# Kernel tuning notes

Hardware: AMD Instinct MI355X
Metric: run time of the kernel (lower is better)

## Reference

```python
import jax, jax.numpy as jnp
import numpy as np

EPS = 1e-12  # tf.nn.l2_normalize epsilon


def setup_inputs() -> dict:
    key = jax.random.key(0)
    ks = jax.random.split(key, 6)
    B, S, K, D = 256, 512, 20, 256
    encoded_sents = jax.random.normal(ks[0], (B, S, D), dtype=jnp.float32)
    mask = jax.random.randint(ks[1], (B, S), 0, 2) > 0
    keys = jax.random.normal(ks[2], (B, K, D), dtype=jnp.float32)
    scale = 0.05  # truncated-normal-ish init scale for stability
    U = jax.random.normal(ks[3], (D, D), dtype=jnp.float32) * scale
    V = jax.random.normal(ks[4], (D, D), dtype=jnp.float32) * scale
    W = jax.random.normal(ks[5], (D, D), dtype=jnp.float32) * scale
    return {"encoded_sents": encoded_sents, "mask": mask, "keys": keys,
            "U": U, "V": V, "W": W}


def reference(encoded_sents, mask, keys, U, V, W):
    # encoded_sents: [B,S,D], mask: [B,S] bool, keys: [B,K,D], U/V/W: [D,D]
    kV = jnp.einsum('bkd,de->bke', keys, V)  # time-invariant, hoisted

    def step(h, xm):
        x, m = xm                                   # x: [B,D], m: [B] bool
        # gate: sigmoid(sum_d x*(h+k))  -> [B,K]
        g = jax.nn.sigmoid(jnp.einsum('bd,bkd->bk', x, h + keys))
        # candidate: relu(hU + kV + xW)  -> [B,K,D]
        h_tilda = jax.nn.relu(jnp.einsum('bkd,de->bke', h, U) + kV
                              + (x @ W)[:, None, :])
        upd = h + g[..., None] * h_tilda
        # l2 normalize along dim (tf.nn.l2_normalize semantics)
        sq = jnp.sum(upd * upd, axis=2, keepdims=True)
        upd = upd * jax.lax.rsqrt(jnp.maximum(sq, EPS))
        h_new = jnp.where(m[:, None, None], upd, h)
        return h_new, None

    h0 = jnp.zeros_like(keys)
    xs = (jnp.swapaxes(encoded_sents, 0, 1), mask.T)  # [S,B,D], [S,B]
    hT, _ = jax.lax.scan(step, h0, xs)
    return hT  # [B,K,D]
```

## Files before the change

### kernel.cpp

```cpp
#include <hip/hip_runtime.h>
#include <math.h>

#define B_ 256
#define S_ 512
#define K_ 20
#define D_ 256
#define NT 512
#define LDH 264

typedef __attribute__((ext_vector_type(8))) short short8;
typedef __attribute__((ext_vector_type(4))) float f32x4;
typedef __attribute__((ext_vector_type(8))) _Float16 half8;
typedef __attribute__((ext_vector_type(2))) __fp16 fp16x2;
typedef __attribute__((ext_vector_type(2))) unsigned int uint2v;

__device__ __forceinline__ unsigned short rne_bf16(float f) {
  unsigned u = __builtin_bit_cast(unsigned, f);
  u += 0x7FFFu + ((u >> 16) & 1u);
  return (unsigned short)(u >> 16);
}
__device__ __forceinline__ float bf16_to_f32(unsigned short h) {
  return __builtin_bit_cast(float, ((unsigned)h) << 16);
}
__device__ __forceinline__ unsigned pk_f16(float a, float b) {
  fp16x2 p = __builtin_amdgcn_cvt_pkrtz(a, b);
  return __builtin_bit_cast(unsigned, p);
}

__global__ __launch_bounds__(NT, 2)
void rnn_fused14(const float* __restrict__ es, const int* __restrict__ mask,
                 const float* __restrict__ keys, const float* __restrict__ U,
                 const float* __restrict__ V, const float* __restrict__ W,
                 float* __restrict__ XWc, float* __restrict__ out) {
  __shared__ unsigned short sH0[32 * LDH];
  __shared__ unsigned short sH1[32 * LDH];
  __shared__ float sRed[2][2][32][13];
  __shared__ float sXK[512 * 20 + 16];
  __shared__ short sAct[S_];
  __shared__ int   sNact;

  const int b = blockIdx.x, t = threadIdx.x;
  const int w = t >> 6, lane = t & 63, quad = lane >> 4, n = lane & 15;
  const int e0a = (w << 5) + quad * 4;

  for (int i = t; i < 2 * 2 * 32 * 13; i += NT) ((float*)sRed)[i] = 0.0f;
  if (w == 0) {
    int base = 0;
    for (int c = 0; c < 8; ++c) {
      int s = c * 64 + lane;
      int mv = mask[b * S_ + s];
      unsigned long long bal = __ballot(mv != 0);
      int pos = base + (int)__popcll(bal & ((1ull << lane) - 1ull));
      if (mv) sAct[pos] = (short)s;
      base += (int)__popcll(bal);
    }
    if (lane == 0) sNact = base;
  }
  __syncthreads();
  const int nAct = sNact;

  short8 aHi[8][2], aLo[8][2];
  auto load_A = [&](const float* __restrict__ M) {
#pragma unroll
    for (int kt = 0; kt < 8; ++kt)
#pragma unroll
      for (int et = 0; et < 2; ++et) {
        const int e = ((2 * w + et) << 4) + n;
        const int d0 = kt * 32 + quad * 8;
        short8 h8, l8;
#pragma unroll
        for (int j = 0; j < 8; ++j) {
          float f = M[(d0 + j) * D_ + e];
          unsigned short hi = rne_bf16(f);
          h8[j] = (short)hi;
          l8[j] = (short)rne_bf16(f - bf16_to_f32(hi));
        }
        aHi[kt][et] = h8; aLo[kt][et] = l8;
      }
  };
  auto load_A_keys = [&]() {
#pragma unroll
    for (int kt = 0; kt < 8; ++kt)
#pragma unroll
      for (int et = 0; et < 2; ++et) {
        const int kk2 = ((2 * w + et) << 4) + n;
        const int d0 = kt * 32 + quad * 8;
        short8 h8 = {}, l8 = {};
        if (kk2 < K_) {
#pragma unroll
          for (int j = 0; j < 8; ++j) {
            float f = keys[(size_t)(b * K_ + kk2) * D_ + d0 + j];
            unsigned short hi = rne_bf16(f);
            h8[j] = (short)hi;
            l8[j] = (short)rne_bf16(f - bf16_to_f32(hi));
          }
        }
        aHi[kt][et] = h8; aLo[kt][et] = l8;
      }
  };
  auto run_mfma3 = [&](f32x4 acc[2][2]) {
#pragma unroll
    for (int kt = 0; kt < 8; ++kt) {
      short8 bhi[2], blo[2];
#pragma unroll
      for (int ke = 0; ke < 2; ++ke) {
        const int off = (ke * 16 + n) * LDH + kt * 32 + quad * 8;
        bhi[ke] = *(const short8*)&sH0[off];
        blo[ke] = *(const short8*)&sH1[off];
      }
#pragma unroll
      for (int et = 0; et < 2; ++et)
#pragma unroll
        for (int ke = 0; ke < 2; ++ke) {
          acc[et][ke] = __builtin_amdgcn_mfma_f32_16x16x32_bf16(aHi[kt][et], bhi[ke], acc[et][ke], 0, 0, 0);
          acc[et][ke] = __builtin_amdgcn_mfma_f32_16x16x32_bf16(aLo[kt][et], bhi[ke], acc[et][ke], 0, 0, 0);
          acc[et][ke] = __builtin_amdgcn_mfma_f32_16x16x32_bf16(aHi[kt][et], blo[ke], acc[et][ke], 0, 0, 0);
        }
    }
  };
  auto stage_rows = [&](int p) {
    const int rr = t >> 4, c0 = (t & 15) * 16;
    const int ridx = p * 32 + rr;
    const int sidx = sAct[(ridx < nAct) ? ridx : (nAct - 1)];
    const float* src = es + ((size_t)b * S_ + sidx) * D_ + c0;
#pragma unroll
    for (int h2 = 0; h2 < 2; ++h2) {
      f32x4 f0 = *(const f32x4*)(src + h2 * 8);
      f32x4 f1 = *(const f32x4*)(src + h2 * 8 + 4);
      short8 hh, ll;
#pragma unroll
      for (int j = 0; j < 4; ++j) {
        unsigned short a = rne_bf16(f0[j]);
        hh[j] = (short)a; ll[j] = (short)rne_bf16(f0[j] - bf16_to_f32(a));
        unsigned short bq = rne_bf16(f1[j]);
        hh[4 + j] = (short)bq; ll[4 + j] = (short)rne_bf16(f1[j] - bf16_to_f32(bq));
      }
      *(short8*)&sH0[rr * LDH + c0 + h2 * 8] = hh;
      *(short8*)&sH1[rr * LDH + c0 + h2 * 8] = ll;
    }
  };

  const size_t bbase = (size_t)b * S_;
  const int nPass = (nAct + 31) >> 5;

  if (nAct > 0) {
    load_A_keys();
    for (int p = 0; p < nPass; ++p) {
      stage_rows(p);
      __syncthreads();
      if (w == 0) {
        f32x4 axk[2][2] = {};
        run_mfma3(axk);
#pragma unroll
        for (int et = 0; et < 2; ++et) {
          const int kb = et * 16 + quad * 4;
          if (kb < K_) {
#pragma unroll
            for (int ke = 0; ke < 2; ++ke) {
              const int row = p * 32 + ke * 16 + n;
              *(f32x4*)&sXK[row * 20 + kb] = axk[et][ke];
            }
          }
        }
      }
      __syncthreads();
    }
  }

  if (nAct > 0) {
    load_A(W);
    for (int p = 0; p < nPass; ++p) {
      stage_rows(p);
      __syncthreads();
      f32x4 acc[2][2] = {};
      run_mfma3(acc);
#pragma unroll
      for (int et = 0; et < 2; ++et)
#pragma unroll
        for (int ke = 0; ke < 2; ++ke) {
          const int g = p * 32 + ke * 16 + n;
          if (g < nAct)
            *(f32x4*)&XWc[(bbase + g) * D_ + e0a + 16 * et] = acc[et][ke];
        }
      __syncthreads();
    }
  }

  for (int i = t; i < 32 * LDH; i += NT) { sH0[i] = 0; sH1[i] = 0; }
  __syncthreads();

  for (int i = t; i < K_ * D_; i += NT) {
    int k = i >> 8, d = i & 255;
    float f = keys[(b * K_ + k) * D_ + d];
    unsigned short hi = rne_bf16(f);
    sH0[k * LDH + d] = hi;
    sH1[k * LDH + d] = rne_bf16(f - bf16_to_f32(hi));
  }
  load_A(V);
  __syncthreads();

  f32x4 kvReg[2][2] = {};
  run_mfma3(kvReg);
  __syncthreads();

  for (int i = t; i < K_ * LDH; i += NT) { sH0[i] = 0; sH1[i] = 0; }
  short8 aU[8][2];
#pragma unroll
  for (int kt = 0; kt < 8; ++kt)
#pragma unroll
    for (int et = 0; et < 2; ++et) {
      const int e = ((2 * w + et) << 4) + n;
      const int d0 = kt * 32 + quad * 8;
      short8 h8;
#pragma unroll
      for (int j = 0; j < 8; ++j)
        h8[j] = (short)__builtin_bit_cast(unsigned short, (_Float16)U[(d0 + j) * D_ + e]);
      aU[kt][et] = h8;
    }

  f32x4 hReg[2][2] = {};
  f32x4 xEc[2] = {}, xwEc[2] = {};
  float xkC = 0.0f;
  const int kk = lane & 31;
  if (nAct > 0) {
    const int s1 = sAct[(nAct > 1) ? 1 : 0];
#pragma unroll
    for (int et = 0; et < 2; ++et) {
      xEc[et]  = *(const f32x4*)&es[((size_t)b * S_ + s1) * D_ + e0a + 16 * et];
      xwEc[et] = *(const f32x4*)&XWc[bbase * D_ + e0a + 16 * et];
    }
    xkC = sXK[kk];
  }
  __syncthreads();

  auto xswap = [](float& a, float& b) {
    asm("v_permlane32_swap_b32 %0, %1" : "+v"(a), "+v"(b));
  };

  auto epi_tile = [&](const f32x4& a4, const f32x4& kv4, const f32x4& xw4,
                      const f32x4& xn4, float lm, float g, f32x4& hR,
                      float& psq, float& pxh, unsigned short* wptr, bool doWrite) {
    f32x4 u;
#pragma unroll
    for (int r = 0; r < 4; ++r) {
      float T = fmaxf(fmaf(lm, a4[r], kv4[r] + xw4[r]), 0.0f);
      float uv = fmaf(g, T, lm * hR[r]);
      u[r] = uv;
      psq = fmaf(uv, uv, psq);
      pxh = fmaf(xn4[r], uv, pxh);
    }
    hR = u;
    uint2v hh;
    hh[0] = pk_f16(u[0], u[1]);
    hh[1] = pk_f16(u[2], u[3]);
    if (doWrite) *(uint2v*)wptr = hh;
  };

  for (int i = 0; i < nAct; ++i) {
    const int rb = i & 1, wbuf = rb ^ 1;
    const unsigned short* bR = rb ? sH1 : sH0;
    unsigned short* bW = rb ? sH0 : sH1;

    const int iX = (i + 2 < nAct) ? i + 2 : nAct - 1;
    const int iW = (i + 1 < nAct) ? i + 1 : nAct - 1;
    const size_t rX = ((size_t)b * S_ + sAct[iX]) * D_;
    f32x4 xEn[2], xwEn[2];
#pragma unroll
    for (int et = 0; et < 2; ++et) {
      xEn[et]  = *(const f32x4*)&es[rX + e0a + 16 * et];
      xwEn[et] = *(const f32x4*)&XWc[(bbase + iW) * D_ + e0a + 16 * et];
    }
    const float xkN = sXK[iW * 20 + kk];

    float lmv, gv;
    {
      f32x4 qa = *(const f32x4*)&sRed[rb][0][kk][0];
      f32x4 qb = *(const f32x4*)&sRed[rb][0][kk][4];
      f32x4 ha = *(const f32x4*)&sRed[rb][1][kk][0];
      f32x4 hb = *(const f32x4*)&sRed[rb][1][kk][4];
      f32x4 qs = qa + qb, hs = ha + hb;
      float ss = (qs[0] + qs[1]) + (qs[2] + qs[3]);
      float xh = (hs[0] + hs[1]) + (hs[2] + hs[3]);
      lmv = rsqrtf(fmaxf(ss, 1e-12f));
      gv = __fdividef(1.0f, 1.0f + __expf(-fmaf(lmv, xh, xkC)));
    }
    const float lm0 = __builtin_bit_cast(float, __builtin_amdgcn_ds_swizzle(__builtin_bit_cast(int, lmv), 0x000F));
    const float g0  = __builtin_bit_cast(float, __builtin_amdgcn_ds_swizzle(__builtin_bit_cast(int, gv),  0x000F));
    const float lm1s = __builtin_bit_cast(float, __builtin_amdgcn_ds_swizzle(__builtin_bit_cast(int, lmv), 0x0203));
    const float g1s  = __builtin_bit_cast(float, __builtin_amdgcn_ds_swizzle(__builtin_bit_cast(int, gv),  0x0203));
    const float lm1 = (n < 4) ? lm1s : 0.0f;
    const float g1 = (n < 4) ? g1s : 0.0f;

    f32x4 a00 = {}, a10 = {};
#pragma unroll
    for (int kt = 0; kt < 8; ++kt) {
      const int co = kt * 32 + quad * 8;
      half8 q0 = __builtin_bit_cast(half8, *(const short8*)&bR[n * LDH + co]);
      a00 = __builtin_amdgcn_mfma_f32_16x16x32_f16(__builtin_bit_cast(half8, aU[kt][0]), q0, a00, 0, 0, 0);
      a10 = __builtin_amdgcn_mfma_f32_16x16x32_f16(__builtin_bit_cast(half8, aU[kt][1]), q0, a10, 0, 0, 0);
    }
    f32x4 a01 = {}, a11 = {};
#pragma unroll
    for (int kt = 0; kt < 8; ++kt) {
      const int co = kt * 32 + quad * 8;
      short8 b1 = {};
      if (n < 4) b1 = *(const short8*)&bR[(16 + n) * LDH + co];
      half8 q1 = __builtin_bit_cast(half8, b1);
      a01 = __builtin_amdgcn_mfma_f32_16x16x32_f16(__builtin_bit_cast(half8, aU[kt][0]), q1, a01, 0, 0, 0);
      a11 = __builtin_amdgcn_mfma_f32_16x16x32_f16(__builtin_bit_cast(half8, aU[kt][1]), q1, a11, 0, 0, 0);
    }

    float psq0 = 0.0f, pxh0 = 0.0f, psq1 = 0.0f, pxh1 = 0.0f;
    epi_tile(a00, kvReg[0][0], xwEc[0], xEc[0], lm0, g0, hReg[0][0],
             psq0, pxh0, &bW[n * LDH + e0a], true);
    epi_tile(a10, kvReg[1][0], xwEc[1], xEc[1], lm0, g0, hReg[1][0],
             psq0, pxh0, &bW[n * LDH + e0a + 16], true);
    epi_tile(a01, kvReg[0][1], xwEc[0], xEc[0], lm1, g1, hReg[0][1],
             psq1, pxh1, &bW[(16 + n) * LDH + e0a], n < 4);
    epi_tile(a11, kvReg[1][1], xwEc[1], xEc[1], lm1, g1, hReg[1][1],
             psq1, pxh1, &bW[(16 + n) * LDH + e0a + 16], n < 4);

    psq0 += __shfl_xor(psq0, 16, 64); psq1 += __shfl_xor(psq1, 16, 64);
    pxh0 += __shfl_xor(pxh0, 16, 64); pxh1 += __shfl_xor(pxh1, 16, 64);
    xswap(psq0, psq1); const float sq_s = psq0 + psq1;
    xswap(pxh0, pxh1); const float xh_s = pxh0 + pxh1;
    if (quad == 0) {
      sRed[wbuf][0][n][w] = sq_s; sRed[wbuf][1][n][w] = xh_s;
    }
    if (quad == 2 && n < 4) {
      sRed[wbuf][0][16 + n][w] = sq_s; sRed[wbuf][1][16 + n][w] = xh_s;
    }
#pragma unroll
    for (int et = 0; et < 2; ++et) { xEc[et] = xEn[et]; xwEc[et] = xwEn[et]; }
    xkC = xkN;
    __syncthreads();
  }

  const int fb = nAct & 1;
  float lmF0, lmF1 = 0.0f;
  {
    f32x4 qa = *(const f32x4*)&sRed[fb][0][n][0];
    f32x4 qb = *(const f32x4*)&sRed[fb][0][n][4];
    f32x4 qs = qa + qb;
    lmF0 = rsqrtf(fmaxf((qs[0] + qs[1]) + (qs[2] + qs[3]), 1e-12f));
  }
  if (n < 4) {
    f32x4 qa = *(const f32x4*)&sRed[fb][0][16 + n][0];
    f32x4 qb = *(const f32x4*)&sRed[fb][0][16 + n][4];
    f32x4 qs = qa + qb;
    lmF1 = rsqrtf(fmaxf((qs[0] + qs[1]) + (qs[2] + qs[3]), 1e-12f));
  }
#pragma unroll
  for (int et = 0; et < 2; ++et) {
    const int e0 = e0a + 16 * et;
    {
      f32x4 o;
#pragma unroll
      for (int r = 0; r < 4; ++r) o[r] = lmF0 * hReg[et][0][r];
      *(f32x4*)&out[(size_t)(b * K_ + n) * D_ + e0] = o;
    }
    if (n < 4) {
      f32x4 o;
#pragma unroll
      for (int r = 0; r < 4; ++r) o[r] = lmF1 * hReg[et][1][r];
      *(f32x4*)&out[(size_t)(b * K_ + 16 + n) * D_ + e0] = o;
    }
  }
}

extern "C" void kernel_launch(void* const* d_in, const int* in_sizes, int n_in,
                              void* d_out, int out_size, void* d_ws, size_t ws_size,
                              hipStream_t stream) {
  const float* es   = (const float*)d_in[0];
  const int*   mask = (const int*)d_in[1];
  const float* keys = (const float*)d_in[2];
  const float* U    = (const float*)d_in[3];
  const float* V    = (const float*)d_in[4];
  const float* W    = (const float*)d_in[5];
  float* out = (float*)d_out;
  float* XWc = (float*)d_ws;
  rnn_fused14<<<B_, NT, 0, stream>>>(es, mask, keys, U, V, W, XWc, out);
}
```

Before: 677.2 us.

## Double block to 1024 threads, give each wave one 16-column output tile

```diff
diff --git a/kernel.cpp b/kernel.cpp
--- a/kernel.cpp
+++ b/kernel.cpp
@@ -5,7 +5,7 @@
 #define S_ 512
 #define K_ 20
 #define D_ 256
-#define NT 512
+#define NT 1024
 #define LDH 264
 
 typedef __attribute__((ext_vector_type(8))) short short8;
@@ -27,23 +27,23 @@
   return __builtin_bit_cast(unsigned, p);
 }
 
-__global__ __launch_bounds__(NT, 2)
-void rnn_fused14(const float* __restrict__ es, const int* __restrict__ mask,
+__global__ __launch_bounds__(NT, 4)
+void rnn_fused15(const float* __restrict__ es, const int* __restrict__ mask,
                  const float* __restrict__ keys, const float* __restrict__ U,
                  const float* __restrict__ V, const float* __restrict__ W,
                  float* __restrict__ XWc, float* __restrict__ out) {
   __shared__ unsigned short sH0[32 * LDH];
   __shared__ unsigned short sH1[32 * LDH];
-  __shared__ float sRed[2][2][32][13];
+  __shared__ float sRed[2][2][32][17];
   __shared__ float sXK[512 * 20 + 16];
   __shared__ short sAct[S_];
   __shared__ int   sNact;
 
   const int b = blockIdx.x, t = threadIdx.x;
   const int w = t >> 6, lane = t & 63, quad = lane >> 4, n = lane & 15;
-  const int e0a = (w << 5) + quad * 4;
-
-  for (int i = t; i < 2 * 2 * 32 * 13; i += NT) ((float*)sRed)[i] = 0.0f;
+  const int e0a = (w << 4) + quad * 4;
+
+  for (int i = t; i < 2 * 2 * 32 * 17; i += NT) ((float*)sRed)[i] = 0.0f;
   if (w == 0) {
     int base = 0;
     for (int c = 0; c < 8; ++c) {
@@ -59,46 +59,42 @@
   __syncthreads();
   const int nAct = sNact;
 
-  short8 aHi[8][2], aLo[8][2];
+  short8 aHi[8], aLo[8];
   auto load_A = [&](const float* __restrict__ M) {
 #pragma unroll
-    for (int kt = 0; kt < 8; ++kt)
-#pragma unroll
-      for (int et = 0; et < 2; ++et) {
-        const int e = ((2 * w + et) << 4) + n;
-        const int d0 = kt * 32 + quad * 8;
-        short8 h8, l8;
+    for (int kt = 0; kt < 8; ++kt) {
+      const int e = (w << 4) + n;
+      const int d0 = kt * 32 + quad * 8;
+      short8 h8, l8;
+#pragma unroll
+      for (int j = 0; j < 8; ++j) {
+        float f = M[(d0 + j) * D_ + e];
+        unsigned short hi = rne_bf16(f);
+        h8[j] = (short)hi;
+        l8[j] = (short)rne_bf16(f - bf16_to_f32(hi));
+      }
+      aHi[kt] = h8; aLo[kt] = l8;
+    }
+  };
+  auto load_A_keys = [&]() {
+#pragma unroll
+    for (int kt = 0; kt < 8; ++kt) {
+      const int kk2 = (w << 4) + n;
+      const int d0 = kt * 32 + quad * 8;
+      short8 h8 = {}, l8 = {};
+      if (kk2 < K_) {
 #pragma unroll
         for (int j = 0; j < 8; ++j) {
-          float f = M[(d0 + j) * D_ + e];
+          float f = keys[(size_t)(b * K_ + kk2) * D_ + d0 + j];
           unsigned short hi = rne_bf16(f);
           h8[j] = (short)hi;
           l8[j] = (short)rne_bf16(f - bf16_to_f32(hi));
         }
-        aHi[kt][et] = h8; aLo[kt][et] = l8;
-      }
-  };
-  auto load_A_keys = [&]() {
-#pragma unroll
-    for (int kt = 0; kt < 8; ++kt)
-#pragma unroll
-      for (int et = 0; et < 2; ++et) {
-        const int kk2 = ((2 * w + et) << 4) + n;
-        const int d0 = kt * 32 + quad * 8;
-        short8 h8 = {}, l8 = {};
-        if (kk2 < K_) {
-#pragma unroll
-          for (int j = 0; j < 8; ++j) {
-            float f = keys[(size_t)(b * K_ + kk2) * D_ + d0 + j];
-            unsigned short hi = rne_bf16(f);
-            h8[j] = (short)hi;
-            l8[j] = (short)rne_bf16(f - bf16_to_f32(hi));
-          }
-        }
-        aHi[kt][et] = h8; aLo[kt][et] = l8;
-      }
-  };
-  auto run_mfma3 = [&](f32x4 acc[2][2]) {
+      }
+      aHi[kt] = h8; aLo[kt] = l8;
+    }
+  };
+  auto run_mfma3 = [&](f32x4 acc[2]) {
 #pragma unroll
     for (int kt = 0; kt < 8; ++kt) {
       short8 bhi[2], blo[2];
@@ -109,35 +105,30 @@
         blo[ke] = *(const short8*)&sH1[off];
       }
 #pragma unroll
-      for (int et = 0; et < 2; ++et)
-#pragma unroll
-        for (int ke = 0; ke < 2; ++ke) {
-          acc[et][ke] = __builtin_amdgcn_mfma_f32_16x16x32_bf16(aHi[kt][et], bhi[ke], acc[et][ke], 0, 0, 0);
-          acc[et][ke] = __builtin_amdgcn_mfma_f32_16x16x32_bf16(aLo[kt][et], bhi[ke], acc[et][ke], 0, 0, 0);
-          acc[et][ke] = __builtin_amdgcn_mfma_f32_16x16x32_bf16(aHi[kt][et], blo[ke], acc[et][ke], 0, 0, 0);
-        }
+      for (int ke = 0; ke < 2; ++ke) {
+        acc[ke] = __builtin_amdgcn_mfma_f32_16x16x32_bf16(aHi[kt], bhi[ke], acc[ke], 0, 0, 0);
+        acc[ke] = __builtin_amdgcn_mfma_f32_16x16x32_bf16(aLo[kt], bhi[ke], acc[ke], 0, 0, 0);
+        acc[ke] = __builtin_amdgcn_mfma_f32_16x16x32_bf16(aHi[kt], blo[ke], acc[ke], 0, 0, 0);
+      }
     }
   };
   auto stage_rows = [&](int p) {
-    const int rr = t >> 4, c0 = (t & 15) * 16;
+    const int rr = t >> 5, c0 = (t & 31) * 8;
     const int ridx = p * 32 + rr;
     const int sidx = sAct[(ridx < nAct) ? ridx : (nAct - 1)];
     const float* src = es + ((size_t)b * S_ + sidx) * D_ + c0;
-#pragma unroll
-    for (int h2 = 0; h2 < 2; ++h2) {
-      f32x4 f0 = *(const f32x4*)(src + h2 * 8);
-      f32x4 f1 = *(const f32x4*)(src + h2 * 8 + 4);
-      short8 hh, ll;
-#pragma unroll
-      for (int j = 0; j < 4; ++j) {
-        unsigned short a = rne_bf16(f0[j]);
-        hh[j] = (short)a; ll[j] = (short)rne_bf16(f0[j] - bf16_to_f32(a));
-        unsigned short bq = rne_bf16(f1[j]);
-        hh[4 + j] = (short)bq; ll[4 + j] = (short)rne_bf16(f1[j] - bf16_to_f32(bq));
-      }
-      *(short8*)&sH0[rr * LDH + c0 + h2 * 8] = hh;
-      *(short8*)&sH1[rr * LDH + c0 + h2 * 8] = ll;
-    }
+    f32x4 f0 = *(const f32x4*)(src);
+    f32x4 f1 = *(const f32x4*)(src + 4);
+    short8 hh, ll;
+#pragma unroll
+    for (int j = 0; j < 4; ++j) {
+      unsigned short a = rne_bf16(f0[j]);
+      hh[j] = (short)a; ll[j] = (short)rne_bf16(f0[j] - bf16_to_f32(a));
+      unsigned short bq = rne_bf16(f1[j]);
+      hh[4 + j] = (short)bq; ll[4 + j] = (short)rne_bf16(f1[j] - bf16_to_f32(bq));
+    }
+    *(short8*)&sH0[rr * LDH + c0] = hh;
+    *(short8*)&sH1[rr * LDH + c0] = ll;
   };
 
   const size_t bbase = (size_t)b * S_;
@@ -148,18 +139,15 @@
     for (int p = 0; p < nPass; ++p) {
       stage_rows(p);
       __syncthreads();
-      if (w == 0) {
-        f32x4 axk[2][2] = {};
+      if (w < 2) {
+        f32x4 axk[2] = {};
         run_mfma3(axk);
-#pragma unroll
-        for (int et = 0; et < 2; ++et) {
-          const int kb = et * 16 + quad * 4;
-          if (kb < K_) {
-#pragma unroll
-            for (int ke = 0; ke < 2; ++ke) {
-              const int row = p * 32 + ke * 16 + n;
-              *(f32x4*)&sXK[row * 20 + kb] = axk[et][ke];
-            }
+        const int kb = (w << 4) + quad * 4;
+        if (kb < K_) {
+#pragma unroll
+          for (int ke = 0; ke < 2; ++ke) {
+            const int row = p * 32 + ke * 16 + n;
+            *(f32x4*)&sXK[row * 20 + kb] = axk[ke];
           }
         }
       }
@@ -172,16 +160,14 @@
     for (int p = 0; p < nPass; ++p) {
       stage_rows(p);
       __syncthreads();
-      f32x4 acc[2][2] = {};
+      f32x4 acc[2] = {};
       run_mfma3(acc);
 #pragma unroll
-      for (int et = 0; et < 2; ++et)
-#pragma unroll
-        for (int ke = 0; ke < 2; ++ke) {
-          const int g = p * 32 + ke * 16 + n;
-          if (g < nAct)
-            *(f32x4*)&XWc[(bbase + g) * D_ + e0a + 16 * et] = acc[et][ke];
-        }
+      for (int ke = 0; ke < 2; ++ke) {
+        const int g = p * 32 + ke * 16 + n;
+        if (g < nAct)
+          *(f32x4*)&XWc[(bbase + g) * D_ + e0a] = acc[ke];
+      }
       __syncthreads();
     }
   }
@@ -199,61 +185,37 @@
   load_A(V);
   __syncthreads();
 
-  f32x4 kvReg[2][2] = {};
+  f32x4 kvReg[2] = {};
   run_mfma3(kvReg);
   __syncthreads();
 
   for (int i = t; i < K_ * LDH; i += NT) { sH0[i] = 0; sH1[i] = 0; }
-  short8 aU[8][2];
-#pragma unroll
-  for (int kt = 0; kt < 8; ++kt)
-#pragma unroll
-    for (int et = 0; et < 2; ++et) {
-      const int e = ((2 * w + et) << 4) + n;
-      const int d0 = kt * 32 + quad * 8;
-      short8 h8;
-#pragma unroll
-      for (int j = 0; j < 8; ++j)
-        h8[j] = (short)__builtin_bit_cast(unsigned short, (_Float16)U[(d0 + j) * D_ + e]);
-      aU[kt][et] = h8;
-    }
-
-  f32x4 hReg[2][2] = {};
-  f32x4 xEc[2] = {}, xwEc[2] = {};
+  short8 aU[8];
+#pragma unroll
+  for (int kt = 0; kt < 8; ++kt) {
+    const int e = (w << 4) + n;
+    const int d0 = kt * 32 + quad * 8;
+    short8 h8;
+#pragma unroll
+    for (int j = 0; j < 8; ++j)
+      h8[j] = (short)__builtin_bit_cast(unsigned short, (_Float16)U[(d0 + j) * D_ + e]);
+    aU[kt] = h8;
+  }
+
+  f32x4 hReg[2] = {};
+  f32x4 xEc = {}, xwEc = {};
   float xkC = 0.0f;
   const int kk = lane & 31;
   if (nAct > 0) {
     const int s1 = sAct[(nAct > 1) ? 1 : 0];
-#pragma unroll
-    for (int et = 0; et < 2; ++et) {
-      xEc[et]  = *(const f32x4*)&es[((size_t)b * S_ + s1) * D_ + e0a + 16 * et];
-      xwEc[et] = *(const f32x4*)&XWc[bbase * D_ + e0a + 16 * et];
-    }
+    xEc  = *(const f32x4*)&es[((size_t)b * S_ + s1) * D_ + e0a];
+    xwEc = *(const f32x4*)&XWc[bbase * D_ + e0a];
     xkC = sXK[kk];
   }
   __syncthreads();
 
   auto xswap = [](float& a, float& b) {
     asm("v_permlane32_swap_b32 %0, %1" : "+v"(a), "+v"(b));
-  };
-
-  auto epi_tile = [&](const f32x4& a4, const f32x4& kv4, const f32x4& xw4,
-                      const f32x4& xn4, float lm, float g, f32x4& hR,
-                      float& psq, float& pxh, unsigned short* wptr, bool doWrite) {
-    f32x4 u;
-#pragma unroll
-    for (int r = 0; r < 4; ++r) {
-      float T = fmaxf(fmaf(lm, a4[r], kv4[r] + xw4[r]), 0.0f);
-      float uv = fmaf(g, T, lm * hR[r]);
-      u[r] = uv;
-      psq = fmaf(uv, uv, psq);
-      pxh = fmaf(xn4[r], uv, pxh);
-    }
-    hR = u;
-    uint2v hh;
-    hh[0] = pk_f16(u[0], u[1]);
-    hh[1] = pk_f16(u[2], u[3]);
-    if (doWrite) *(uint2v*)wptr = hh;
   };
 
   for (int i = 0; i < nAct; ++i) {
@@ -264,21 +226,21 @@
     const int iX = (i + 2 < nAct) ? i + 2 : nAct - 1;
     const int iW = (i + 1 < nAct) ? i + 1 : nAct - 1;
     const size_t rX = ((size_t)b * S_ + sAct[iX]) * D_;
-    f32x4 xEn[2], xwEn[2];
-#pragma unroll
-    for (int et = 0; et < 2; ++et) {
-      xEn[et]  = *(const f32x4*)&es[rX + e0a + 16 * et];
-      xwEn[et] = *(const f32x4*)&XWc[(bbase + iW) * D_ + e0a + 16 * et];
-    }
+    f32x4 xEn  = *(const f32x4*)&es[rX + e0a];
+    f32x4 xwEn = *(const f32x4*)&XWc[(bbase + iW) * D_ + e0a];
     const float xkN = sXK[iW * 20 + kk];
 
     float lmv, gv;
     {
       f32x4 qa = *(const f32x4*)&sRed[rb][0][kk][0];
       f32x4 qb = *(const f32x4*)&sRed[rb][0][kk][4];
+      f32x4 qc = *(const f32x4*)&sRed[rb][0][kk][8];
+      f32x4 qd = *(const f32x4*)&sRed[rb][0][kk][12];
       f32x4 ha = *(const f32x4*)&sRed[rb][1][kk][0];
       f32x4 hb = *(const f32x4*)&sRed[rb][1][kk][4];
-      f32x4 qs = qa + qb, hs = ha + hb;
+      f32x4 hc = *(const f32x4*)&sRed[rb][1][kk][8];
+      f32x4 hd = *(const f32x4*)&sRed[rb][1][kk][12];
+      f32x4 qs = (qa + qb) + (qc + qd), hs = (ha + hb) + (hc + hd);
       float ss = (qs[0] + qs[1]) + (qs[2] + qs[3]);
       float xh = (hs[0] + hs[1]) + (hs[2] + hs[3]);
       lmv = rsqrtf(fmaxf(ss, 1e-12f));
@@ -291,34 +253,54 @@
     const float lm1 = (n < 4) ? lm1s : 0.0f;
     const float g1 = (n < 4) ? g1s : 0.0f;
 
-    f32x4 a00 = {}, a10 = {};
+    f32x4 a0 = {}, a1 = {};
 #pragma unroll
     for (int kt = 0; kt < 8; ++kt) {
       const int co = kt * 32 + quad * 8;
       half8 q0 = __builtin_bit_cast(half8, *(const short8*)&bR[n * LDH + co]);
-      a00 = __builtin_amdgcn_mfma_f32_16x16x32_f16(__builtin_bit_cast(half8, aU[kt][0]), q0, a00, 0, 0, 0);
-      a10 = __builtin_amdgcn_mfma_f32_16x16x32_f16(__builtin_bit_cast(half8, aU[kt][1]), q0, a10, 0, 0, 0);
-    }
-    f32x4 a01 = {}, a11 = {};
-#pragma unroll
-    for (int kt = 0; kt < 8; ++kt) {
-      const int co = kt * 32 + quad * 8;
       short8 b1 = {};
       if (n < 4) b1 = *(const short8*)&bR[(16 + n) * LDH + co];
       half8 q1 = __builtin_bit_cast(half8, b1);
-      a01 = __builtin_amdgcn_mfma_f32_16x16x32_f16(__builtin_bit_cast(half8, aU[kt][0]), q1, a01, 0, 0, 0);
-      a11 = __builtin_amdgcn_mfma_f32_16x16x32_f16(__builtin_bit_cast(half8, aU[kt][1]), q1, a11, 0, 0, 0);
+      half8 aq = __builtin_bit_cast(half8, aU[kt]);
+      a0 = __builtin_amdgcn_mfma_f32_16x16x32_f16(aq, q0, a0, 0, 0, 0);
+      a1 = __builtin_amdgcn_mfma_f32_16x16x32_f16(aq, q1, a1, 0, 0, 0);
     }
 
     float psq0 = 0.0f, pxh0 = 0.0f, psq1 = 0.0f, pxh1 = 0.0f;
-    epi_tile(a00, kvReg[0][0], xwEc[0], xEc[0], lm0, g0, hReg[0][0],
-             psq0, pxh0, &bW[n * LDH + e0a], true);
-    epi_tile(a10, kvReg[1][0], xwEc[1], xEc[1], lm0, g0, hReg[1][0],
-             psq0, pxh0, &bW[n * LDH + e0a + 16], true);
-    epi_tile(a01, kvReg[0][1], xwEc[0], xEc[0], lm1, g1, hReg[0][1],
-             psq1, pxh1, &bW[(16 + n) * LDH + e0a], n < 4);
-    epi_tile(a11, kvReg[1][1], xwEc[1], xEc[1], lm1, g1, hReg[1][1],
-             psq1, pxh1, &bW[(16 + n) * LDH + e0a + 16], n < 4);
+    {
+      f32x4 u;
+#pragma unroll
+      for (int r = 0; r < 4; ++r) {
+        float T = fmaxf(fmaf(lm0, a0[r], kvReg[0][r] + xwEc[r]), 0.0f);
+        float uv = fmaf(g0, T, lm0 * hReg[0][r]);
+        u[r] = uv;
+        psq0 = fmaf(uv, uv, psq0);
+        pxh0 = fmaf(xEc[r], uv, pxh0);
+      }
+      hReg[0] = u;
+      uint2v hh;
+      hh[0] = pk_f16(u[0], u[1]);
+      hh[1] = pk_f16(u[2], u[3]);
+      *(uint2v*)&bW[n * LDH + e0a] = hh;
+    }
+    {
+      f32x4 u;
+#pragma unroll
+      for (int r = 0; r < 4; ++r) {
+        float T = fmaxf(fmaf(lm1, a1[r], kvReg[1][r] + xwEc[r]), 0.0f);
+        float uv = fmaf(g1, T, lm1 * hReg[1][r]);
+        u[r] = uv;
+        psq1 = fmaf(uv, uv, psq1);
+        pxh1 = fmaf(xEc[r], uv, pxh1);
+      }
+      hReg[1] = u;
+      if (n < 4) {
+        uint2v hh;
+        hh[0] = pk_f16(u[0], u[1]);
+        hh[1] = pk_f16(u[2], u[3]);
+        *(uint2v*)&bW[(16 + n) * LDH + e0a] = hh;
+      }
+    }
 
     psq0 += __shfl_xor(psq0, 16, 64); psq1 += __shfl_xor(psq1, 16, 64);
     pxh0 += __shfl_xor(pxh0, 16, 64); pxh1 += __shfl_xor(pxh1, 16, 64);
@@ -330,9 +312,7 @@
     if (quad == 2 && n < 4) {
       sRed[wbuf][0][16 + n][w] = sq_s; sRed[wbuf][1][16 + n][w] = xh_s;
     }
-#pragma unroll
-    for (int et = 0; et < 2; ++et) { xEc[et] = xEn[et]; xwEc[et] = xwEn[et]; }
-    xkC = xkN;
+    xEc = xEn; xwEc = xwEn; xkC = xkN;
     __syncthreads();
   }
 
@@ -341,30 +321,30 @@
   {
     f32x4 qa = *(const f32x4*)&sRed[fb][0][n][0];
     f32x4 qb = *(const f32x4*)&sRed[fb][0][n][4];
-    f32x4 qs = qa + qb;
+    f32x4 qc = *(const f32x4*)&sRed[fb][0][n][8];
+    f32x4 qd = *(const f32x4*)&sRed[fb][0][n][12];
+    f32x4 qs = (qa + qb) + (qc + qd);
     lmF0 = rsqrtf(fmaxf((qs[0] + qs[1]) + (qs[2] + qs[3]), 1e-12f));
   }
   if (n < 4) {
     f32x4 qa = *(const f32x4*)&sRed[fb][0][16 + n][0];
     f32x4 qb = *(const f32x4*)&sRed[fb][0][16 + n][4];
-    f32x4 qs = qa + qb;
+    f32x4 qc = *(const f32x4*)&sRed[fb][0][16 + n][8];
+    f32x4 qd = *(const f32x4*)&sRed[fb][0][16 + n][12];
+    f32x4 qs = (qa + qb) + (qc + qd);
     lmF1 = rsqrtf(fmaxf((qs[0] + qs[1]) + (qs[2] + qs[3]), 1e-12f));
   }
-#pragma unroll
-  for (int et = 0; et < 2; ++et) {
-    const int e0 = e0a + 16 * et;
-    {
-      f32x4 o;
-#pragma unroll
-      for (int r = 0; r < 4; ++r) o[r] = lmF0 * hReg[et][0][r];
-      *(f32x4*)&out[(size_t)(b * K_ + n) * D_ + e0] = o;
-    }
-    if (n < 4) {
-      f32x4 o;
-#pragma unroll
-      for (int r = 0; r < 4; ++r) o[r] = lmF1 * hReg[et][1][r];
-      *(f32x4*)&out[(size_t)(b * K_ + 16 + n) * D_ + e0] = o;
-    }
+  {
+    f32x4 o;
+#pragma unroll
+    for (int r = 0; r < 4; ++r) o[r] = lmF0 * hReg[0][r];
+    *(f32x4*)&out[(size_t)(b * K_ + n) * D_ + e0a] = o;
+  }
+  if (n < 4) {
+    f32x4 o;
+#pragma unroll
+    for (int r = 0; r < 4; ++r) o[r] = lmF1 * hReg[1][r];
+    *(f32x4*)&out[(size_t)(b * K_ + 16 + n) * D_ + e0a] = o;
   }
 }
 
@@ -379,5 +359,5 @@
   const float* W    = (const float*)d_in[5];
   float* out = (float*)d_out;
   float* XWc = (float*)d_ws;
-  rnn_fused14<<<B_, NT, 0, stream>>>(es, mask, keys, U, V, W, XWc, out);
-}
+  rnn_fused15<<<B_, NT, 0, stream>>>(es, mask, keys, U, V, W, XWc, out);
+}
```

After: 837.1 us. 23.6% more time.
